# Optimization experiments

Measured on AMD Instinct MI355X. Metric: run time of the kernel, lower is better.

## Reference

```python
import jax, jax.numpy as jnp
import numpy as np

N = 100000      # num_nodes
E = 6400000     # num edges
D = 128         # embedding_dim
R = 8           # num_roles
ALPHA = 0.15
ITERS = 10

def setup_inputs() -> dict:
    key = jax.random.key(0)
    k1, k2, k3, k4, k5 = jax.random.split(key, 5)
    edge_index = jax.random.randint(k1, (2, E), 0, N)
    batch_nodes = jax.random.randint(k2, (N,), 0, N)
    importance_emb = jax.random.normal(k3, (N, D), dtype=jnp.float32)
    resizer_W = jax.random.normal(k4, (D, 2), dtype=jnp.float32) * (1.0 / np.sqrt(D))
    resizer_b = jnp.zeros((2,), dtype=jnp.float32)
    # xavier_uniform for behavior_matrix [R, 4]
    limit = np.sqrt(6.0 / (R + 4))
    behavior_matrix = jax.random.uniform(k5, (R, 4), minval=-limit, maxval=limit, dtype=jnp.float32)
    return {
        'edge_index': edge_index,
        'batch_nodes': batch_nodes,
        'importance_emb': importance_emb,
        'resizer_W': resizer_W,
        'resizer_b': resizer_b,
        'behavior_matrix': behavior_matrix,
    }

def reference(edge_index, batch_nodes, importance_emb, resizer_W, resizer_b, behavior_matrix):
    src, dst = edge_index[0], edge_index[1]
    num_edges = src.shape[0]
    # out-degrees via segment_sum (== bincount)
    out_deg = jax.ops.segment_sum(jnp.ones((num_edges,), jnp.float32), src, num_segments=N)
    inv_deg_src = 1.0 / jnp.maximum(out_deg, 1.0)[src]  # [E], clamp(min=1)

    # approximate_pagerank: 10 iterations of gather -> scale -> scatter_add
    def body(pr, _):
        contrib = (1.0 - ALPHA) * pr[src] * inv_deg_src
        new_pr = jax.ops.segment_sum(contrib, dst, num_segments=N) + ALPHA / N
        return new_pr, None
    pr0 = jnp.full((N,), 1.0 / N, dtype=jnp.float32)
    pagerank, _ = jax.lax.scan(body, pr0, None, length=ITERS)

    # resizer: single Linear(D, 2)
    emb2 = importance_emb @ resizer_W + resizer_b  # [B, 2]

    # X = [deg[batch], pagerank[batch], emb2] -> [B, 4]
    X = jnp.concatenate([out_deg[batch_nodes][:, None],
                         pagerank[batch_nodes][:, None],
                         emb2], axis=1)

    # lstsq(H.T, X.T): A = H.T is [4, R], underdetermined -> minimum-norm
    # solution Z = A^T (A A^T)^{-1} X^T ; W = Z^T  -> [B, R]
    A = behavior_matrix.T                      # [4, R]
    G = A @ A.T                                # [4, 4]
    W = (A.T @ jnp.linalg.solve(G, X.T)).T     # [B, R]

    # F.normalize(W, p=2, dim=1)
    norm = jnp.linalg.norm(W, axis=1, keepdims=True)
    roles = W / jnp.maximum(norm, 1e-12)
    return roles
```

## Files before the change

### kernel.cpp

```cpp
#include <hip/hip_runtime.h>
#include <math.h>

#define N_NODES 100000
#define N_EDGES 6400000
#define DIM     128
#define NROLES  8
#define ALPHA   0.15f
#define PR_ITERS 10

#define BUCKET_SHIFT 9
#define BUCKET_SIZE  512
#define NBUCKET      196
#define NB2          392
#define NBLK_BIN     256
#define CHUNK        25000

__global__ void k_prep_M(const float* __restrict__ H, float* __restrict__ Mout) {
    if (threadIdx.x != 0 || blockIdx.x != 0) return;
    double G[4][4];
    for (int i = 0; i < 4; ++i)
        for (int j = 0; j < 4; ++j) {
            double s = 0.0;
            for (int r = 0; r < NROLES; ++r)
                s += (double)H[r * 4 + i] * (double)H[r * 4 + j];
            G[i][j] = s;
        }
    double aug[4][8];
    for (int i = 0; i < 4; ++i)
        for (int j = 0; j < 4; ++j) {
            aug[i][j] = G[i][j];
            aug[i][j + 4] = (i == j) ? 1.0 : 0.0;
        }
    for (int c = 0; c < 4; ++c) {
        int p = c; double best = fabs(aug[c][c]);
        for (int r = c + 1; r < 4; ++r) {
            double v = fabs(aug[r][c]);
            if (v > best) { best = v; p = r; }
        }
        if (p != c)
            for (int j = 0; j < 8; ++j) {
                double t = aug[c][j]; aug[c][j] = aug[p][j]; aug[p][j] = t;
            }
        double piv = aug[c][c];
        for (int j = 0; j < 8; ++j) aug[c][j] /= piv;
        for (int r = 0; r < 4; ++r) {
            if (r == c) continue;
            double f = aug[r][c];
            for (int j = 0; j < 8; ++j) aug[r][j] -= f * aug[c][j];
        }
    }
    for (int r = 0; r < NROLES; ++r)
        for (int k = 0; k < 4; ++k) {
            double s = 0.0;
            for (int j = 0; j < 4; ++j)
                s += (double)H[r * 4 + j] * aug[j][k + 4];
            Mout[r * 4 + k] = (float)s;
        }
}

__global__ __launch_bounds__(256)
void k_hist(const int* __restrict__ src, const int* __restrict__ dst,
            unsigned* __restrict__ counts) {
    __shared__ unsigned h[NB2];
    for (int i = threadIdx.x; i < NB2; i += 256) h[i] = 0;
    __syncthreads();
    int beg = blockIdx.x * CHUNK;
    int t = threadIdx.x;
    int mainEnd = beg + 24576;
    for (int e = beg + t * 4; e < mainEnd; e += 1024) {
        int4 s4 = *(const int4*)(src + e);
        int4 d4 = *(const int4*)(dst + e);
        atomicAdd(&h[((unsigned)d4.x) >> BUCKET_SHIFT], 1u);
        atomicAdd(&h[((unsigned)d4.y) >> BUCKET_SHIFT], 1u);
        atomicAdd(&h[((unsigned)d4.z) >> BUCKET_SHIFT], 1u);
        atomicAdd(&h[((unsigned)d4.w) >> BUCKET_SHIFT], 1u);
        atomicAdd(&h[NBUCKET + (((unsigned)s4.x) >> BUCKET_SHIFT)], 1u);
        atomicAdd(&h[NBUCKET + (((unsigned)s4.y) >> BUCKET_SHIFT)], 1u);
        atomicAdd(&h[NBUCKET + (((unsigned)s4.z) >> BUCKET_SHIFT)], 1u);
        atomicAdd(&h[NBUCKET + (((unsigned)s4.w) >> BUCKET_SHIFT)], 1u);
    }
    for (int e = mainEnd + t; e < beg + CHUNK; e += 256) {
        atomicAdd(&h[((unsigned)dst[e]) >> BUCKET_SHIFT], 1u);
        atomicAdd(&h[NBUCKET + (((unsigned)src[e]) >> BUCKET_SHIFT)], 1u);
    }
    __syncthreads();
    for (int i = threadIdx.x; i < NB2; i += 256)
        counts[blockIdx.x * NB2 + i] = h[i];
}

__global__ __launch_bounds__(256)
void k_scanA(const unsigned* __restrict__ counts, unsigned* __restrict__ offs,
             unsigned* __restrict__ btot) {
    int bucket = blockIdx.x, t = threadIdx.x, lane = t & 63, wv = t >> 6;
    unsigned v = counts[t * NB2 + bucket], x = v;
    #pragma unroll
    for (int o = 1; o < 64; o <<= 1) {
        unsigned y = __shfl_up(x, o);
        if (lane >= o) x += y;
    }
    __shared__ unsigned wsum[4];
    if (lane == 63) wsum[wv] = x;
    __syncthreads();
    unsigned carry = 0;
    for (int w = 0; w < wv; ++w) carry += wsum[w];
    x += carry;
    offs[t * NB2 + bucket] = x - v;
    if (t == 255) btot[bucket] = x;
}

__global__ __launch_bounds__(256)
void k_scanB(const unsigned* __restrict__ btot, unsigned* __restrict__ bases) {
    int half = blockIdx.x;
    int t = threadIdx.x, lane = t & 63, wv = t >> 6;
    unsigned v = (t < NBUCKET) ? btot[half * NBUCKET + t] : 0u, x = v;
    #pragma unroll
    for (int o = 1; o < 64; o <<= 1) {
        unsigned y = __shfl_up(x, o);
        if (lane >= o) x += y;
    }
    __shared__ unsigned wsum[4];
    if (lane == 63) wsum[wv] = x;
    __syncthreads();
    unsigned carry = 0;
    for (int w = 0; w < wv; ++w) carry += wsum[w];
    x += carry;
    if (t <= NBUCKET) bases[half * 256 + t] = x - v;
}

__global__ __launch_bounds__(256)
void k_place(const int* __restrict__ src, const int* __restrict__ dst,
             const unsigned* __restrict__ offs, const unsigned* __restrict__ bases,
             unsigned* __restrict__ rec, unsigned short* __restrict__ recs) {
    __shared__ unsigned cD[NBUCKET];
    __shared__ unsigned cS[NBUCKET];
    for (int i = threadIdx.x; i < NBUCKET; i += 256) {
        cD[i] = bases[i]       + offs[blockIdx.x * NB2 + i];
        cS[i] = bases[256 + i] + offs[blockIdx.x * NB2 + NBUCKET + i];
    }
    __syncthreads();
    int beg = blockIdx.x * CHUNK;
    int t = threadIdx.x;
    int mainEnd = beg + 24576;
    for (int e = beg + t * 4; e < mainEnd; e += 1024) {
        int4 s4 = *(const int4*)(src + e);
        int4 d4 = *(const int4*)(dst + e);
        #pragma unroll
        for (int k = 0; k < 4; ++k) {
            unsigned s = (unsigned)((&s4.x)[k]);
            unsigned d = (unsigned)((&d4.x)[k]);
            unsigned pos = atomicAdd(&cD[d >> BUCKET_SHIFT], 1u);
            rec[pos] = ((d & (BUCKET_SIZE - 1)) << 17) | s;
            unsigned pos2 = atomicAdd(&cS[s >> BUCKET_SHIFT], 1u);
            recs[pos2] = (unsigned short)(s & (BUCKET_SIZE - 1));
        }
    }
    for (int e = mainEnd + t; e < beg + CHUNK; e += 256) {
        unsigned s = (unsigned)src[e];
        unsigned d = (unsigned)dst[e];
        unsigned pos = atomicAdd(&cD[d >> BUCKET_SHIFT], 1u);
        rec[pos] = ((d & (BUCKET_SIZE - 1)) << 17) | s;
        unsigned pos2 = atomicAdd(&cS[s >> BUCKET_SHIFT], 1u);
        recs[pos2] = (unsigned short)(s & (BUCKET_SIZE - 1));
    }
}

__global__ __launch_bounds__(256)
void k_count_init(const unsigned short* __restrict__ recs,
                  const unsigned* __restrict__ bases,
                  float* __restrict__ deg, float* __restrict__ s,
                  float* __restrict__ val0) {
    __shared__ unsigned cnt[BUCKET_SIZE];
    int t = threadIdx.x;
    cnt[t] = 0; cnt[t + 256] = 0;
    __syncthreads();
    int b = blockIdx.x;
    unsigned st = bases[256 + b], en = bases[256 + b + 1];
    unsigned a = (st + 7u) & ~7u;
    if (a > en) a = en;
    for (unsigned i = st + t; i < a; i += 256)
        atomicAdd(&cnt[recs[i]], 1u);
    unsigned mainN = (en - a) & ~2047u;
    const uint4* rp = (const uint4*)(recs + a);
    for (unsigned i = t; i * 8u < mainN; i += 256) {
        uint4 r = rp[i];
        atomicAdd(&cnt[r.x & 0xFFFFu], 1u); atomicAdd(&cnt[r.x >> 16], 1u);
        atomicAdd(&cnt[r.y & 0xFFFFu], 1u); atomicAdd(&cnt[r.y >> 16], 1u);
        atomicAdd(&cnt[r.z & 0xFFFFu], 1u); atomicAdd(&cnt[r.z >> 16], 1u);
        atomicAdd(&cnt[r.w & 0xFFFFu], 1u); atomicAdd(&cnt[r.w >> 16], 1u);
    }
    for (unsigned i = a + mainN + t; i < en; i += 256)
        atomicAdd(&cnt[recs[i]], 1u);
    __syncthreads();
    #pragma unroll
    for (int k = 0; k < 2; ++k) {
        int v = b * BUCKET_SIZE + t + k * 256;
        if (v < N_NODES) {
            float d = (float)cnt[t + k * 256];
            float sv = (1.0f - ALPHA) / fmaxf(d, 1.0f);
            deg[v] = d;
            s[v] = sv;
            val0[v] = sv * (1.0f / (float)N_NODES);
        }
    }
}

__global__ __launch_bounds__(256)
void k_iter(const unsigned* __restrict__ rec, const unsigned* __restrict__ bases,
            const float* __restrict__ val, const float* __restrict__ s,
            float* __restrict__ pr, float* __restrict__ valn) {
    __shared__ float acc[BUCKET_SIZE];
    int t = threadIdx.x;
    acc[t] = 0.0f;
    acc[t + 256] = 0.0f;
    __syncthreads();
    int b = blockIdx.x;
    unsigned st = bases[b], en = bases[b + 1], n = en - st;
    unsigned mainN = n & ~1023u;
    for (unsigned i = t; i < mainN; i += 1024) {
        unsigned r0 = rec[st + i];
        unsigned r1 = rec[st + i + 256];
        unsigned r2 = rec[st + i + 512];
        unsigned r3 = rec[st + i + 768];
        float v0 = val[r0 & 0x1FFFFu];
        float v1 = val[r1 & 0x1FFFFu];
        float v2 = val[r2 & 0x1FFFFu];
        float v3 = val[r3 & 0x1FFFFu];
        atomicAdd(&acc[r0 >> 17], v0);
        atomicAdd(&acc[r1 >> 17], v1);
        atomicAdd(&acc[r2 >> 17], v2);
        atomicAdd(&acc[r3 >> 17], v3);
    }
    for (unsigned i = mainN + t; i < n; i += 256) {
        unsigned r = rec[st + i];
        atomicAdd(&acc[r >> 17], val[r & 0x1FFFFu]);
    }
    __syncthreads();
    #pragma unroll
    for (int k = 0; k < 2; ++k) {
        int v = b * BUCKET_SIZE + t + k * 256;
        if (v < N_NODES) {
            float p = acc[t + k * 256] + ALPHA / (float)N_NODES;
            pr[v] = p;
            valn[v] = p * s[v];
        }
    }
}

__global__ __launch_bounds__(256)
void k_final(const float* __restrict__ emb, const float* __restrict__ rW,
             const float* __restrict__ rb, const int* __restrict__ batch,
             const float* __restrict__ deg, const float* __restrict__ pr,
             const float* __restrict__ M, float* __restrict__ out) {
    int wid  = (blockIdx.x * blockDim.x + threadIdx.x) >> 6;
    int lane = threadIdx.x & 63;
    if (wid >= N_NODES) return;

    const float* row = emb + (size_t)wid * DIM;
    float e0 = row[lane];
    float e1 = row[lane + 64];
    float2 w0 = ((const float2*)rW)[lane];
    float2 w1 = ((const float2*)rW)[lane + 64];
    float a0 = e0 * w0.x + e1 * w1.x;
    float a1 = e0 * w0.y + e1 * w1.y;
    #pragma unroll
    for (int off = 32; off; off >>= 1) {
        a0 += __shfl_xor(a0, off);
        a1 += __shfl_xor(a1, off);
    }

    int bn = batch[wid];
    float x0 = deg[bn];
    float x1 = pr[bn];
    float x2 = a0 + rb[0];
    float x3 = a1 + rb[1];

    float wr = 0.0f;
    if (lane < NROLES) {
        const float* m = M + lane * 4;
        wr = m[0] * x0 + m[1] * x1 + m[2] * x2 + m[3] * x3;
    }
    float sq = wr * wr;
    #pragma unroll
    for (int off = 4; off; off >>= 1) sq += __shfl_xor(sq, off);
    float inv = 1.0f / fmaxf(sqrtf(sq), 1e-12f);
    if (lane < NROLES) out[(size_t)wid * NROLES + lane] = wr * inv;
}

extern "C" void kernel_launch(void* const* d_in, const int* in_sizes, int n_in,
                              void* d_out, int out_size, void* d_ws, size_t ws_size,
                              hipStream_t stream) {
    const int*   edge  = (const int*)d_in[0];
    const int*   src   = edge;
    const int*   dst   = edge + N_EDGES;
    const int*   batch = (const int*)d_in[1];
    const float* emb   = (const float*)d_in[2];
    const float* rW    = (const float*)d_in[3];
    const float* rb    = (const float*)d_in[4];
    const float* H     = (const float*)d_in[5];
    float*       out   = (float*)d_out;

    float*    deg    = (float*)d_ws;
    float*    s      = deg   + 100352;
    float*    pr     = s     + 100352;
    float*    valA   = pr    + 100352;
    float*    valB   = valA  + 100352;
    float*    M      = valB  + 100352;
    unsigned* counts = (unsigned*)(M + 32);
    unsigned* offs   = counts + NBLK_BIN * NB2;
    unsigned* btot   = offs   + NBLK_BIN * NB2;
    unsigned* bases  = btot   + 512;
    unsigned* rec    = bases  + 512;
    unsigned short* recs = (unsigned short*)(rec + N_EDGES);

    k_prep_M<<<1, 1, 0, stream>>>(H, M);

    k_hist <<<NBLK_BIN, 256, 0, stream>>>(src, dst, counts);
    k_scanA<<<NB2,      256, 0, stream>>>(counts, offs, btot);
    k_scanB<<<2,        256, 0, stream>>>(btot, bases);
    k_place<<<NBLK_BIN, 256, 0, stream>>>(src, dst, offs, bases, rec, recs);
    k_count_init<<<NBUCKET, 256, 0, stream>>>(recs, bases, deg, s, valA);

    float* vcur = valA;
    float* vnxt = valB;
    for (int it = 0; it < PR_ITERS; ++it) {
        k_iter<<<NBUCKET, 256, 0, stream>>>(rec, bases, vcur, s, pr, vnxt);
        float* t = vcur; vcur = vnxt; vnxt = t;
    }

    const int FG = (N_NODES + 3) / 4;
    k_final<<<FG, 256, 0, stream>>>(emb, rW, rb, batch, deg, pr, M, out);
}
```

Measured before the change: 573.7 us.

## Split PageRank bucket edges across segments with partial sums and reduce kernel

```diff
diff --git a/kernel.cpp b/kernel.cpp
--- a/kernel.cpp
+++ b/kernel.cpp
@@ -14,6 +14,7 @@
 #define NB2          392
 #define NBLK_BIN     256
 #define CHUNK        25000
+#define SEG          8
 
 __global__ void k_prep_M(const float* __restrict__ H, float* __restrict__ Mout) {
     if (threadIdx.x != 0 || blockIdx.x != 0) return;
@@ -205,45 +206,60 @@
 }
 
 __global__ __launch_bounds__(256)
-void k_iter(const unsigned* __restrict__ rec, const unsigned* __restrict__ bases,
-            const float* __restrict__ val, const float* __restrict__ s,
-            float* __restrict__ pr, float* __restrict__ valn) {
+void k_iter2(const unsigned* __restrict__ rec, const unsigned* __restrict__ bases,
+             const float* __restrict__ val, float* __restrict__ partial) {
     __shared__ float acc[BUCKET_SIZE];
     int t = threadIdx.x;
     acc[t] = 0.0f;
     acc[t + 256] = 0.0f;
     __syncthreads();
-    int b = blockIdx.x;
+    int b   = blockIdx.x >> 3;
+    int seg = blockIdx.x & 7;
     unsigned st = bases[b], en = bases[b + 1], n = en - st;
-    unsigned mainN = n & ~1023u;
-    for (unsigned i = t; i < mainN; i += 1024) {
-        unsigned r0 = rec[st + i];
-        unsigned r1 = rec[st + i + 256];
-        unsigned r2 = rec[st + i + 512];
-        unsigned r3 = rec[st + i + 768];
-        float v0 = val[r0 & 0x1FFFFu];
-        float v1 = val[r1 & 0x1FFFFu];
-        float v2 = val[r2 & 0x1FFFFu];
-        float v3 = val[r3 & 0x1FFFFu];
-        atomicAdd(&acc[r0 >> 17], v0);
-        atomicAdd(&acc[r1 >> 17], v1);
-        atomicAdd(&acc[r2 >> 17], v2);
-        atomicAdd(&acc[r3 >> 17], v3);
-    }
-    for (unsigned i = mainN + t; i < n; i += 256) {
-        unsigned r = rec[st + i];
+    unsigned s0 = st + (unsigned)(((unsigned long long)n * (unsigned)seg) >> 3);
+    unsigned s1 = st + (unsigned)(((unsigned long long)n * (unsigned)(seg + 1)) >> 3);
+    unsigned a0 = (s0 + 3u) & ~3u;
+    if (a0 > s1) a0 = s1;
+    for (unsigned i = s0 + t; i < a0; i += 256) {
+        unsigned r = rec[i];
         atomicAdd(&acc[r >> 17], val[r & 0x1FFFFu]);
     }
-    __syncthreads();
-    #pragma unroll
-    for (int k = 0; k < 2; ++k) {
-        int v = b * BUCKET_SIZE + t + k * 256;
-        if (v < N_NODES) {
-            float p = acc[t + k * 256] + ALPHA / (float)N_NODES;
-            pr[v] = p;
-            valn[v] = p * s[v];
-        }
-    }
+    unsigned nv = (s1 - a0) >> 2;
+    const uint4* rp = (const uint4*)(rec + a0);
+    for (unsigned i = t; i < nv; i += 256) {
+        uint4 r = rp[i];
+        float v0 = val[r.x & 0x1FFFFu];
+        float v1 = val[r.y & 0x1FFFFu];
+        float v2 = val[r.z & 0x1FFFFu];
+        float v3 = val[r.w & 0x1FFFFu];
+        atomicAdd(&acc[r.x >> 17], v0);
+        atomicAdd(&acc[r.y >> 17], v1);
+        atomicAdd(&acc[r.z >> 17], v2);
+        atomicAdd(&acc[r.w >> 17], v3);
+    }
+    for (unsigned i = a0 + nv * 4u + t; i < s1; i += 256) {
+        unsigned r = rec[i];
+        atomicAdd(&acc[r >> 17], val[r & 0x1FFFFu]);
+    }
+    __syncthreads();
+    float* p = partial + ((unsigned)blockIdx.x << 9);
+    p[t] = acc[t];
+    p[t + 256] = acc[t + 256];
+}
+
+__global__ __launch_bounds__(256)
+void k_reduce(const float* __restrict__ partial, const float* __restrict__ s,
+              float* __restrict__ pr, float* __restrict__ valn) {
+    int v = blockIdx.x * 256 + threadIdx.x;
+    if (v >= N_NODES) return;
+    int b = v >> BUCKET_SHIFT, local = v & (BUCKET_SIZE - 1);
+    const float* p = partial + ((unsigned)(b * SEG) << 9) + local;
+    float sum = 0.0f;
+    #pragma unroll
+    for (int k = 0; k < SEG; ++k) sum += p[k << 9];
+    float pv = sum + ALPHA / (float)N_NODES;
+    pr[v] = pv;
+    valn[v] = pv * s[v];
 }
 
 __global__ __launch_bounds__(256)
@@ -311,6 +327,7 @@
     unsigned* bases  = btot   + 512;
     unsigned* rec    = bases  + 512;
     unsigned short* recs = (unsigned short*)(rec + N_EDGES);
+    float*    partial = (float*)(recs + N_EDGES);
 
     k_prep_M<<<1, 1, 0, stream>>>(H, M);
 
@@ -323,7 +340,8 @@
     float* vcur = valA;
     float* vnxt = valB;
     for (int it = 0; it < PR_ITERS; ++it) {
-        k_iter<<<NBUCKET, 256, 0, stream>>>(rec, bases, vcur, s, pr, vnxt);
+        k_iter2 <<<NBUCKET * SEG, 256, 0, stream>>>(rec, bases, vcur, partial);
+        k_reduce<<<(N_NODES + 255) / 256, 256, 0, stream>>>(partial, s, pr, vnxt);
         float* t = vcur; vcur = vnxt; vnxt = t;
     }
 
```

Measured after the change: 541.6 us. 1.06x faster.

## Sort dst buckets by source bin and compress PageRank edge records to 16-bit

Applied to the files above, without the earlier changes.

```diff
diff --git a/kernel.cpp b/kernel.cpp
--- a/kernel.cpp
+++ b/kernel.cpp
@@ -8,12 +8,17 @@
 #define ALPHA   0.15f
 #define PR_ITERS 10
 
-#define BUCKET_SHIFT 9
-#define BUCKET_SIZE  512
-#define NBUCKET      196
-#define NB2          392
-#define NBLK_BIN     256
-#define CHUNK        25000
+#define DSH      8
+#define DBS      256
+#define NDB      391
+#define SSH      9
+#define SBS      512
+#define NSB      196
+#define NBT      587
+#define NBLK_BIN 256
+#define CHUNK    25000
+#define NBIN     391
+#define CAP16    24576
 
 __global__ void k_prep_M(const float* __restrict__ H, float* __restrict__ Mout) {
     if (threadIdx.x != 0 || blockIdx.x != 0) return;
@@ -61,8 +66,8 @@
 __global__ __launch_bounds__(256)
 void k_hist(const int* __restrict__ src, const int* __restrict__ dst,
             unsigned* __restrict__ counts) {
-    __shared__ unsigned h[NB2];
-    for (int i = threadIdx.x; i < NB2; i += 256) h[i] = 0;
+    __shared__ unsigned h[NBT];
+    for (int i = threadIdx.x; i < NBT; i += 256) h[i] = 0;
     __syncthreads();
     int beg = blockIdx.x * CHUNK;
     int t = threadIdx.x;
@@ -70,29 +75,29 @@
     for (int e = beg + t * 4; e < mainEnd; e += 1024) {
         int4 s4 = *(const int4*)(src + e);
         int4 d4 = *(const int4*)(dst + e);
-        atomicAdd(&h[((unsigned)d4.x) >> BUCKET_SHIFT], 1u);
-        atomicAdd(&h[((unsigned)d4.y) >> BUCKET_SHIFT], 1u);
-        atomicAdd(&h[((unsigned)d4.z) >> BUCKET_SHIFT], 1u);
-        atomicAdd(&h[((unsigned)d4.w) >> BUCKET_SHIFT], 1u);
-        atomicAdd(&h[NBUCKET + (((unsigned)s4.x) >> BUCKET_SHIFT)], 1u);
-        atomicAdd(&h[NBUCKET + (((unsigned)s4.y) >> BUCKET_SHIFT)], 1u);
-        atomicAdd(&h[NBUCKET + (((unsigned)s4.z) >> BUCKET_SHIFT)], 1u);
-        atomicAdd(&h[NBUCKET + (((unsigned)s4.w) >> BUCKET_SHIFT)], 1u);
+        atomicAdd(&h[((unsigned)d4.x) >> DSH], 1u);
+        atomicAdd(&h[((unsigned)d4.y) >> DSH], 1u);
+        atomicAdd(&h[((unsigned)d4.z) >> DSH], 1u);
+        atomicAdd(&h[((unsigned)d4.w) >> DSH], 1u);
+        atomicAdd(&h[NDB + (((unsigned)s4.x) >> SSH)], 1u);
+        atomicAdd(&h[NDB + (((unsigned)s4.y) >> SSH)], 1u);
+        atomicAdd(&h[NDB + (((unsigned)s4.z) >> SSH)], 1u);
+        atomicAdd(&h[NDB + (((unsigned)s4.w) >> SSH)], 1u);
     }
     for (int e = mainEnd + t; e < beg + CHUNK; e += 256) {
-        atomicAdd(&h[((unsigned)dst[e]) >> BUCKET_SHIFT], 1u);
-        atomicAdd(&h[NBUCKET + (((unsigned)src[e]) >> BUCKET_SHIFT)], 1u);
-    }
-    __syncthreads();
-    for (int i = threadIdx.x; i < NB2; i += 256)
-        counts[blockIdx.x * NB2 + i] = h[i];
+        atomicAdd(&h[((unsigned)dst[e]) >> DSH], 1u);
+        atomicAdd(&h[NDB + (((unsigned)src[e]) >> SSH)], 1u);
+    }
+    __syncthreads();
+    for (int i = threadIdx.x; i < NBT; i += 256)
+        counts[blockIdx.x * NBT + i] = h[i];
 }
 
 __global__ __launch_bounds__(256)
 void k_scanA(const unsigned* __restrict__ counts, unsigned* __restrict__ offs,
              unsigned* __restrict__ btot) {
     int bucket = blockIdx.x, t = threadIdx.x, lane = t & 63, wv = t >> 6;
-    unsigned v = counts[t * NB2 + bucket], x = v;
+    unsigned v = counts[t * NBT + bucket], x = v;
     #pragma unroll
     for (int o = 1; o < 64; o <<= 1) {
         unsigned y = __shfl_up(x, o);
@@ -104,39 +109,40 @@
     unsigned carry = 0;
     for (int w = 0; w < wv; ++w) carry += wsum[w];
     x += carry;
-    offs[t * NB2 + bucket] = x - v;
+    offs[t * NBT + bucket] = x - v;
     if (t == 255) btot[bucket] = x;
 }
 
-__global__ __launch_bounds__(256)
+__global__ __launch_bounds__(512)
 void k_scanB(const unsigned* __restrict__ btot, unsigned* __restrict__ bases) {
     int half = blockIdx.x;
+    int len  = half ? NSB : NDB;
     int t = threadIdx.x, lane = t & 63, wv = t >> 6;
-    unsigned v = (t < NBUCKET) ? btot[half * NBUCKET + t] : 0u, x = v;
+    unsigned v = (t < len) ? btot[(half ? NDB : 0) + t] : 0u, x = v;
     #pragma unroll
     for (int o = 1; o < 64; o <<= 1) {
         unsigned y = __shfl_up(x, o);
         if (lane >= o) x += y;
     }
-    __shared__ unsigned wsum[4];
+    __shared__ unsigned wsum[8];
     if (lane == 63) wsum[wv] = x;
     __syncthreads();
     unsigned carry = 0;
     for (int w = 0; w < wv; ++w) carry += wsum[w];
     x += carry;
-    if (t <= NBUCKET) bases[half * 256 + t] = x - v;
+    if (t <= len) bases[half * 512 + t] = x - v;
 }
 
 __global__ __launch_bounds__(256)
 void k_place(const int* __restrict__ src, const int* __restrict__ dst,
              const unsigned* __restrict__ offs, const unsigned* __restrict__ bases,
              unsigned* __restrict__ rec, unsigned short* __restrict__ recs) {
-    __shared__ unsigned cD[NBUCKET];
-    __shared__ unsigned cS[NBUCKET];
-    for (int i = threadIdx.x; i < NBUCKET; i += 256) {
-        cD[i] = bases[i]       + offs[blockIdx.x * NB2 + i];
-        cS[i] = bases[256 + i] + offs[blockIdx.x * NB2 + NBUCKET + i];
-    }
+    __shared__ unsigned cD[NDB];
+    __shared__ unsigned cS[NSB];
+    for (int i = threadIdx.x; i < NDB; i += 256)
+        cD[i] = bases[i] + offs[blockIdx.x * NBT + i];
+    for (int i = threadIdx.x; i < NSB; i += 256)
+        cS[i] = bases[512 + i] + offs[blockIdx.x * NBT + NDB + i];
     __syncthreads();
     int beg = blockIdx.x * CHUNK;
     int t = threadIdx.x;
@@ -148,19 +154,19 @@
         for (int k = 0; k < 4; ++k) {
             unsigned s = (unsigned)((&s4.x)[k]);
             unsigned d = (unsigned)((&d4.x)[k]);
-            unsigned pos = atomicAdd(&cD[d >> BUCKET_SHIFT], 1u);
-            rec[pos] = ((d & (BUCKET_SIZE - 1)) << 17) | s;
-            unsigned pos2 = atomicAdd(&cS[s >> BUCKET_SHIFT], 1u);
-            recs[pos2] = (unsigned short)(s & (BUCKET_SIZE - 1));
+            unsigned pos = atomicAdd(&cD[d >> DSH], 1u);
+            rec[pos] = ((d & (DBS - 1)) << 17) | s;
+            unsigned pos2 = atomicAdd(&cS[s >> SSH], 1u);
+            recs[pos2] = (unsigned short)(s & (SBS - 1));
         }
     }
     for (int e = mainEnd + t; e < beg + CHUNK; e += 256) {
         unsigned s = (unsigned)src[e];
         unsigned d = (unsigned)dst[e];
-        unsigned pos = atomicAdd(&cD[d >> BUCKET_SHIFT], 1u);
-        rec[pos] = ((d & (BUCKET_SIZE - 1)) << 17) | s;
-        unsigned pos2 = atomicAdd(&cS[s >> BUCKET_SHIFT], 1u);
-        recs[pos2] = (unsigned short)(s & (BUCKET_SIZE - 1));
+        unsigned pos = atomicAdd(&cD[d >> DSH], 1u);
+        rec[pos] = ((d & (DBS - 1)) << 17) | s;
+        unsigned pos2 = atomicAdd(&cS[s >> SSH], 1u);
+        recs[pos2] = (unsigned short)(s & (SBS - 1));
     }
 }
 
@@ -169,12 +175,12 @@
                   const unsigned* __restrict__ bases,
                   float* __restrict__ deg, float* __restrict__ s,
                   float* __restrict__ val0) {
-    __shared__ unsigned cnt[BUCKET_SIZE];
+    __shared__ unsigned cnt[SBS];
     int t = threadIdx.x;
     cnt[t] = 0; cnt[t + 256] = 0;
     __syncthreads();
     int b = blockIdx.x;
-    unsigned st = bases[256 + b], en = bases[256 + b + 1];
+    unsigned st = bases[512 + b], en = bases[512 + b + 1];
     unsigned a = (st + 7u) & ~7u;
     if (a > en) a = en;
     for (unsigned i = st + t; i < a; i += 256)
@@ -193,7 +199,7 @@
     __syncthreads();
     #pragma unroll
     for (int k = 0; k < 2; ++k) {
-        int v = b * BUCKET_SIZE + t + k * 256;
+        int v = b * SBS + t + k * 256;
         if (v < N_NODES) {
             float d = (float)cnt[t + k * 256];
             float sv = (1.0f - ALPHA) / fmaxf(d, 1.0f);
@@ -205,43 +211,117 @@
 }
 
 __global__ __launch_bounds__(256)
-void k_iter(const unsigned* __restrict__ rec, const unsigned* __restrict__ bases,
-            const float* __restrict__ val, const float* __restrict__ s,
-            float* __restrict__ pr, float* __restrict__ valn) {
-    __shared__ float acc[BUCKET_SIZE];
+void k_sort2(const unsigned* __restrict__ rec, const unsigned* __restrict__ bases,
+             unsigned short* __restrict__ rec16, unsigned* __restrict__ tabG) {
+    __shared__ unsigned cur[NBIN];
+    __shared__ unsigned tabL[NBIN + 1];
+    __shared__ unsigned wsum2[4];
+    __shared__ unsigned short buf[CAP16];
+    int t = threadIdx.x, lane = t & 63, wv = t >> 6;
+    int b = blockIdx.x;
+    unsigned st = bases[b], en = bases[b + 1];
+    for (int i = t; i < NBIN; i += 256) cur[i] = 0;
+    __syncthreads();
+    for (unsigned i = st + t; i < en; i += 256)
+        atomicAdd(&cur[(rec[i] & 0x1FFFFu) >> 8], 1u);
+    __syncthreads();
+    unsigned loc0 = 0, loc1 = 0, sum = 0;
+    if (2 * t < NBIN)     loc0 = cur[2 * t];
+    if (2 * t + 1 < NBIN) loc1 = cur[2 * t + 1];
+    sum = loc0 + loc1;
+    unsigned x = sum;
+    #pragma unroll
+    for (int o = 1; o < 64; o <<= 1) {
+        unsigned y = __shfl_up(x, o);
+        if (lane >= o) x += y;
+    }
+    if (lane == 63) wsum2[wv] = x;
+    __syncthreads();
+    unsigned carry = 0;
+    for (int w = 0; w < wv; ++w) carry += wsum2[w];
+    unsigned base = carry + x - sum;
+    if (2 * t <= NBIN)     tabL[2 * t] = base;
+    if (2 * t + 1 <= NBIN) tabL[2 * t + 1] = base + loc0;
+    __syncthreads();
+    for (int i = t; i < NBIN; i += 256) cur[i] = tabL[i];
+    __syncthreads();
+    for (unsigned i = st + t; i < en; i += 256) {
+        unsigned r = rec[i];
+        unsigned bin = (r & 0x1FFFFu) >> 8;
+        unsigned p = atomicAdd(&cur[bin], 1u);
+        buf[p] = (unsigned short)(((r >> 17) << 8) | (r & 255u));
+    }
+    __syncthreads();
+    unsigned n = tabL[NBIN];
+    unsigned* gout = (unsigned*)(rec16 + (size_t)b * CAP16);
+    const unsigned* bin32 = (const unsigned*)buf;
+    unsigned nw = (n + 1u) >> 1;
+    for (unsigned i = t; i < nw; i += 256) gout[i] = bin32[i];
+    for (int i = t; i <= NBIN; i += 256) tabG[b * (NBIN + 1) + i] = tabL[i];
+}
+
+__global__ __launch_bounds__(512)
+void k_iterV(const unsigned short* __restrict__ rec16,
+             const unsigned* __restrict__ tabG,
+             const float* __restrict__ val, const float* __restrict__ s,
+             float* __restrict__ pr, float* __restrict__ valn) {
+    __shared__ unsigned tab[NBIN + 1];
+    __shared__ float acc[DBS];
     int t = threadIdx.x;
-    acc[t] = 0.0f;
-    acc[t + 256] = 0.0f;
-    __syncthreads();
     int b = blockIdx.x;
-    unsigned st = bases[b], en = bases[b + 1], n = en - st;
-    unsigned mainN = n & ~1023u;
-    for (unsigned i = t; i < mainN; i += 1024) {
-        unsigned r0 = rec[st + i];
-        unsigned r1 = rec[st + i + 256];
-        unsigned r2 = rec[st + i + 512];
-        unsigned r3 = rec[st + i + 768];
-        float v0 = val[r0 & 0x1FFFFu];
-        float v1 = val[r1 & 0x1FFFFu];
-        float v2 = val[r2 & 0x1FFFFu];
-        float v3 = val[r3 & 0x1FFFFu];
-        atomicAdd(&acc[r0 >> 17], v0);
-        atomicAdd(&acc[r1 >> 17], v1);
-        atomicAdd(&acc[r2 >> 17], v2);
-        atomicAdd(&acc[r3 >> 17], v3);
-    }
-    for (unsigned i = mainN + t; i < n; i += 256) {
-        unsigned r = rec[st + i];
-        atomicAdd(&acc[r >> 17], val[r & 0x1FFFFu]);
-    }
-    __syncthreads();
-    #pragma unroll
-    for (int k = 0; k < 2; ++k) {
-        int v = b * BUCKET_SIZE + t + k * 256;
+    if (t <= NBIN) tab[t] = tabG[b * (NBIN + 1) + t];
+    if (t < DBS) acc[t] = 0.0f;
+    __syncthreads();
+    unsigned n = tab[NBIN];
+    unsigned start = (unsigned)(((unsigned long long)n * (unsigned)t) >> 9) & ~7u;
+    unsigned end   = (t == 511) ? n
+                   : ((unsigned)(((unsigned long long)n * (unsigned)(t + 1)) >> 9) & ~7u);
+    const unsigned short* rp = rec16 + (size_t)b * CAP16;
+    unsigned bin = 0;
+    #pragma unroll
+    for (unsigned step = 256; step; step >>= 1) {
+        unsigned nb = bin + step;
+        if (nb <= NBIN - 1 && tab[nb] <= start) bin = nb;
+    }
+    unsigned i = start;
+    for (; i + 8 <= end; i += 8) {
+        uint4 q = *(const uint4*)(rp + i);
+        unsigned r0 = q.x & 0xFFFFu, r1 = q.x >> 16;
+        unsigned r2 = q.y & 0xFFFFu, r3 = q.y >> 16;
+        unsigned r4 = q.z & 0xFFFFu, r5 = q.z >> 16;
+        unsigned r6 = q.w & 0xFFFFu, r7 = q.w >> 16;
+        unsigned s0, s1, s2, s3, s4, s5, s6, s7;
+        while (i + 0 >= tab[bin + 1]) ++bin;  s0 = (bin << 8) + (r0 & 255u);
+        while (i + 1 >= tab[bin + 1]) ++bin;  s1 = (bin << 8) + (r1 & 255u);
+        while (i + 2 >= tab[bin + 1]) ++bin;  s2 = (bin << 8) + (r2 & 255u);
+        while (i + 3 >= tab[bin + 1]) ++bin;  s3 = (bin << 8) + (r3 & 255u);
+        while (i + 4 >= tab[bin + 1]) ++bin;  s4 = (bin << 8) + (r4 & 255u);
+        while (i + 5 >= tab[bin + 1]) ++bin;  s5 = (bin << 8) + (r5 & 255u);
+        while (i + 6 >= tab[bin + 1]) ++bin;  s6 = (bin << 8) + (r6 & 255u);
+        while (i + 7 >= tab[bin + 1]) ++bin;  s7 = (bin << 8) + (r7 & 255u);
+        float v0 = val[s0], v1 = val[s1], v2 = val[s2], v3 = val[s3];
+        float v4 = val[s4], v5 = val[s5], v6 = val[s6], v7 = val[s7];
+        atomicAdd(&acc[r0 >> 8], v0);
+        atomicAdd(&acc[r1 >> 8], v1);
+        atomicAdd(&acc[r2 >> 8], v2);
+        atomicAdd(&acc[r3 >> 8], v3);
+        atomicAdd(&acc[r4 >> 8], v4);
+        atomicAdd(&acc[r5 >> 8], v5);
+        atomicAdd(&acc[r6 >> 8], v6);
+        atomicAdd(&acc[r7 >> 8], v7);
+    }
+    for (; i < end; ++i) {
+        unsigned r = rp[i];
+        while (i >= tab[bin + 1]) ++bin;
+        atomicAdd(&acc[r >> 8], val[(bin << 8) + (r & 255u)]);
+    }
+    __syncthreads();
+    if (t < DBS) {
+        int v = b * DBS + t;
         if (v < N_NODES) {
-            float p = acc[t + k * 256] + ALPHA / (float)N_NODES;
-            pr[v] = p;
-            valn[v] = p * s[v];
+            float pv = acc[t] + ALPHA / (float)N_NODES;
+            pr[v] = pv;
+            valn[v] = pv * s[v];
         }
     }
 }
@@ -306,24 +386,28 @@
     float*    valB   = valA  + 100352;
     float*    M      = valB  + 100352;
     unsigned* counts = (unsigned*)(M + 32);
-    unsigned* offs   = counts + NBLK_BIN * NB2;
-    unsigned* btot   = offs   + NBLK_BIN * NB2;
-    unsigned* bases  = btot   + 512;
-    unsigned* rec    = bases  + 512;
-    unsigned short* recs = (unsigned short*)(rec + N_EDGES);
+    unsigned* offs   = counts + NBLK_BIN * NBT;
+    unsigned* btot   = offs   + NBLK_BIN * NBT;
+    unsigned* bases  = btot   + 1024;
+    unsigned* rec    = bases  + 1024;
+    unsigned short* recs  = (unsigned short*)(rec + N_EDGES);
+    unsigned short* rec16 = recs;
+    unsigned* tabG   = (unsigned*)(rec16 + (size_t)NDB * CAP16);
+    float*    dummy  = (float*)(tabG + NDB * (NBIN + 1)); (void)dummy;
 
     k_prep_M<<<1, 1, 0, stream>>>(H, M);
 
     k_hist <<<NBLK_BIN, 256, 0, stream>>>(src, dst, counts);
-    k_scanA<<<NB2,      256, 0, stream>>>(counts, offs, btot);
-    k_scanB<<<2,        256, 0, stream>>>(btot, bases);
+    k_scanA<<<NBT,      256, 0, stream>>>(counts, offs, btot);
+    k_scanB<<<2,        512, 0, stream>>>(btot, bases);
     k_place<<<NBLK_BIN, 256, 0, stream>>>(src, dst, offs, bases, rec, recs);
-    k_count_init<<<NBUCKET, 256, 0, stream>>>(recs, bases, deg, s, valA);
+    k_count_init<<<NSB, 256, 0, stream>>>(recs, bases, deg, s, valA);
+    k_sort2<<<NDB,      256, 0, stream>>>(rec, bases, rec16, tabG);
 
     float* vcur = valA;
     float* vnxt = valB;
     for (int it = 0; it < PR_ITERS; ++it) {
-        k_iter<<<NBUCKET, 256, 0, stream>>>(rec, bases, vcur, s, pr, vnxt);
+        k_iterV<<<NDB, 512, 0, stream>>>(rec16, tabG, vcur, s, pr, vnxt);
         float* t = vcur; vcur = vnxt; vnxt = t;
     }
 
```

Result: slower. 655.1 us (+14.2%).
